# Kernel optimization log

Hardware: AMD Instinct MI355X
Metric: run time of the kernel (lower is better)

The kernel has to match this reference:

```python
import jax, jax.numpy as jnp
import numpy as np

LMAX = 10
F_IN = 64
F_OUT = 64
N_GRID = 512
IRREP_DIM = sum((2 * l + 1) ** 2 for l in range(LMAX + 1))  # 1771
BATCH = 256


def setup_inputs() -> dict:
    key = jax.random.key(0)
    kx, kD, kw = jax.random.split(key, 3)
    x = jax.random.normal(kx, (BATCH, F_IN, IRREP_DIM), dtype=jnp.float32)
    D = jax.random.normal(kD, (N_GRID, IRREP_DIM), dtype=jnp.float32)
    w = jax.random.normal(kw, (F_IN, F_OUT, N_GRID), dtype=jnp.float32)
    return {"x": x, "D": D, "w": w}


def _so3_linear(x, psi):
    # x:   (B, f_in, sum_l (2l+1)^2) signal over SO(3) irreps
    # psi: (f_in, f_out, sum_l (2l+1)^2) per-degree block weights
    B, f_in, _ = x.shape
    f_out = psi.shape[1]
    outs = []
    off = 0
    for l in range(LMAX + 1):
        d = 2 * l + 1
        blk = d * d
        # input block: multiplicity u (=d) x irrep component m (=d)
        x_l = x[:, :, off:off + blk].reshape(B, f_in, d, d)        # (B,i,u,m)
        w_l = psi[:, :, off:off + blk].reshape(f_in, f_out, d, d)  # (i,o,u,v)
        alpha = 1.0 / np.sqrt(f_in * d)  # e3nn fan-in path normalization
        out_l = jnp.einsum('bium,iouv->bovm', x_l, w_l) * alpha
        outs.append(out_l.reshape(B, f_out, blk))
        off += blk
    return jnp.concatenate(outs, axis=-1)


def reference(x, D, w):
    # project spatial filter into Fourier (irrep) domain
    n_grid = D.shape[0]
    psi = jnp.einsum('ni,xyn->xyi', D, w) / np.sqrt(n_grid)  # (f_in, f_out, IRREP_DIM)
    return _so3_linear(x, psi)
```

## Files before the change

kernel.cpp:

```cpp
#include <hip/hip_runtime.h>
#include <hip/hip_bf16.h>

#define IDIM 1771
#define NF 64
#define NG 512

constexpr int OFFS[12] = {0, 1, 10, 35, 84, 165, 286, 455, 680, 969, 1330, 1771};

typedef float f32x4 __attribute__((ext_vector_type(4)));
typedef float f32x2 __attribute__((ext_vector_type(2)));
typedef __bf16 bf16x2 __attribute__((ext_vector_type(2)));
typedef __bf16 bf16x8 __attribute__((ext_vector_type(8)));

__device__ __forceinline__ void gl_lds16(const void* g, void* l) {
    __builtin_amdgcn_global_load_lds((const __attribute__((address_space(1))) void*)g,
                                     (__attribute__((address_space(3))) void*)l, 16, 0, 0);
}

__global__ __launch_bounds__(256) void prep_repack_kernel(const float* __restrict__ D,
                                                          const float* __restrict__ w,
                                                          const float* __restrict__ x,
                                                          __bf16* __restrict__ Dt,
                                                          __bf16* __restrict__ wb,
                                                          __hip_bfloat16* __restrict__ A) {
    __shared__ alignas(16) char smem[16640];
    const int blk = blockIdx.x;
    const int t = threadIdx.x;
    const int lane = t & 63, grp = t >> 6;

    if (blk < 224) {
        float (*T)[65] = (float (*)[65])smem;
        const int ct = blk >> 3, nt = blk & 7;
        const int c0 = ct * 64, n0 = nt * 64;
        float tmp[16];
#pragma unroll
        for (int p = 0; p < 16; ++p) {
            int nn = grp + p * 4;
            int c = c0 + lane;
            tmp[p] = (c < IDIM) ? D[(size_t)(n0 + nn) * IDIM + c] : 0.0f;
        }
#pragma unroll
        for (int p = 0; p < 16; ++p) T[grp + p * 4][lane] = tmp[p];
        __syncthreads();
        for (int cc = grp; cc < 64; cc += 4) {
            int c = c0 + cc;
            if (c < IDIM) Dt[c * NG + n0 + lane] = (__bf16)T[lane][cc];
        }
    } else if (blk < 288) {
        const int o = blk - 224;
#pragma unroll
        for (int ii0 = 0; ii0 < 64; ii0 += 8) {
            f32x2 tmp[8];
#pragma unroll
            for (int j = 0; j < 8; ++j)
                tmp[j] = *(const f32x2*)&w[((size_t)((ii0 + j) * 64 + o)) * NG + t * 2];
#pragma unroll
            for (int j = 0; j < 8; ++j) {
                bf16x2 ov;
                ov.x = (__bf16)tmp[j].x;
                ov.y = (__bf16)tmp[j].y;
                *(bf16x2*)&wb[((size_t)(o * 64 + ii0 + j)) * NG + t * 2] = ov;
            }
        }
    } else {
        const int idx = blk - 288;
        const int l = idx >> 8;
        const int b = idx & 255;
        const int d = 2 * l + 1, off = OFFS[l], csq = d * d, Kp = 64 * d;
        __bf16 (*T)[66] = (__bf16 (*)[66])smem;
        const float* xb = x + (size_t)b * NF * IDIM + off;
        __bf16* Ab = (__bf16*)(A + (size_t)16384 * off + (size_t)b * d * Kp);

        for (int c0 = 0; c0 < csq; c0 += 64) {
            float tmp[16];
#pragma unroll
            for (int p = 0; p < 16; ++p) {
                int ii = grp + p * 4;
                int c = c0 + lane;
                tmp[p] = (c < csq) ? xb[(size_t)ii * IDIM + c] : 0.0f;
            }
#pragma unroll
            for (int p = 0; p < 16; ++p) T[grp + p * 4][lane] = (__bf16)tmp[p];
            __syncthreads();
#pragma unroll
            for (int s = 0; s < 2; ++s) {
                int idx2 = s * 256 + t;
                int c_loc = idx2 >> 3, i0 = (idx2 & 7) * 8;
                int c = c0 + c_loc;
                if (c < csq) {
                    int u = (unsigned)c / (unsigned)d;
                    int m = c - u * d;
                    bf16x8 v;
#pragma unroll
                    for (int j = 0; j < 8; ++j) v[j] = T[i0 + j][c_loc];
                    *(bf16x8*)(Ab + (size_t)m * Kp + u * 64 + i0) = v;
                }
            }
            __syncthreads();
        }
    }
}

__global__ __launch_bounds__(256) void psi_mfma_kernel(const __bf16* __restrict__ Dt,
                                                       const __bf16* __restrict__ wb,
                                                       __bf16* __restrict__ Bm) {
    __shared__ alignas(16) __bf16 S[3 * 8192];

    const int t = threadIdx.x, w = t >> 6, ln = t & 63;
    const int row0 = blockIdx.x * 128;
    const int col0 = blockIdx.y * 128;

    const __bf16* gp[4];
    __bf16* lp[4];
#pragma unroll
    for (int q = 0; q < 4; ++q) {
        int chunk = w * 4 + q;
        bool isA = chunk < 8;
        int j = chunk & 7;
        int r16 = j * 16 + (ln >> 2);
        int g = isA ? (row0 + r16 < IDIM ? row0 + r16 : IDIM - 1) : (col0 + r16);
        gp[q] = (isA ? Dt : wb) + (size_t)g * NG + (ln & 3) * 8;
        lp[q] = S + (isA ? 0 : 4096) + j * 512;
    }

    f32x4 acc[4][4];
    f32x4 zero = {0.0f, 0.0f, 0.0f, 0.0f};
#pragma unroll
    for (int i = 0; i < 4; ++i)
#pragma unroll
        for (int j = 0; j < 4; ++j) acc[i][j] = zero;

    const int wr = (w >> 1) * 64, wc = (w & 1) * 64;
    const int fr = ln & 15, kh = ln >> 4;

    auto STAGE = [&](int bi) {
#pragma unroll
        for (int q = 0; q < 4; ++q) {
            gl_lds16(gp[q], lp[q] + bi * 8192);
            gp[q] += 32;
        }
    };

    const int nsteps = NG / 32;
    STAGE(0);
    STAGE(1);

    int bi = 0;
    for (int s = 0; s < nsteps; ++s) {
        if (s + 1 < nsteps) asm volatile("s_waitcnt vmcnt(4)" ::: "memory");
        else                asm volatile("s_waitcnt vmcnt(0)" ::: "memory");
        __builtin_amdgcn_s_barrier();
        __builtin_amdgcn_sched_barrier(0);
        if (s + 2 < nsteps) {
            int nb = s + 2 - ((s + 2) >= 3 ? 3 : 0);
            nb = (s + 2) % 3;
            STAGE(nb);
        }
        __builtin_amdgcn_sched_barrier(0);
        const __bf16* As_ = S + bi * 8192;
        const __bf16* Bs_ = S + bi * 8192 + 4096;
        bf16x8 af[4], bfr[4];
#pragma unroll
        for (int mt = 0; mt < 4; ++mt)
            af[mt] = *(const bf16x8*)&As_[(wr + mt * 16 + fr) * 32 + kh * 8];
#pragma unroll
        for (int nt = 0; nt < 4; ++nt)
            bfr[nt] = *(const bf16x8*)&Bs_[(wc + nt * 16 + fr) * 32 + kh * 8];
#pragma unroll
        for (int mt = 0; mt < 4; ++mt)
#pragma unroll
            for (int nt = 0; nt < 4; ++nt)
                acc[mt][nt] = __builtin_amdgcn_mfma_f32_16x16x32_bf16(af[mt], bfr[nt],
                                                                      acc[mt][nt], 0, 0, 0);
        bi = (bi == 2) ? 0 : bi + 1;
    }

    const float sc = 0.04419417382415922f;
    const int o = (col0 + wc) >> 6;
#pragma unroll
    for (int mt = 0; mt < 4; ++mt) {
#pragma unroll
        for (int e = 0; e < 4; ++e) {
            int c = row0 + wr + mt * 16 + kh * 4 + e;
            if (c < IDIM) {
                int l = 0;
#pragma unroll
                for (int ll = 1; ll < 11; ++ll)
                    if (c >= OFFS[ll]) l = ll;
                int d = 2 * l + 1, off = OFFS[l];
                int rem = c - off;
                int u = (unsigned)rem / (unsigned)d;
                int v = rem - u * d;
                __bf16* bb = Bm + (size_t)4096 * off + (size_t)(o * d + v) * (64 * d) + u * 64;
#pragma unroll
                for (int nt = 0; nt < 4; ++nt) {
                    int i = nt * 16 + fr;
                    bb[i] = (__bf16)(acc[mt][nt][e] * sc);
                }
            }
        }
    }
}

__global__ __launch_bounds__(256) void so3_gemm_all(const __bf16* __restrict__ A,
                                                    const __bf16* __restrict__ Bm,
                                                    float* __restrict__ out) {
    const int bid = blockIdx.x;
    const int v_ = (bid & 7) * 237 + (bid >> 3);
    if (v_ >= 1892) return;

    int l = 10, base = 0;
    if (v_ >= 462)  { l = 9; base = 462; }
    if (v_ >= 842)  { l = 8; base = 842; }
    if (v_ >= 1148) { l = 7; base = 1148; }
    if (v_ >= 1388) { l = 6; base = 1388; }
    if (v_ >= 1570) { l = 5; base = 1570; }
    if (v_ >= 1702) { l = 4; base = 1702; }
    if (v_ >= 1792) { l = 3; base = 1792; }
    if (v_ >= 1848) { l = 2; base = 1848; }
    if (v_ >= 1878) { l = 1; base = 1878; }
    if (v_ >= 1890) { l = 0; base = 1890; }

    const int d = 2 * l + 1;
    const int off = OFFS[l];
    const int Np = 64 * d, Kp = 64 * d;
    const int ntiles = l + 1;
    const int rel = v_ - base;
    const int bx = (unsigned)rel / (unsigned)ntiles;
    const int by = rel - bx * ntiles;
    const int row0 = bx * 128, col0 = by * 128;

    constexpr float ALPHA[11] = {0.125f, 0.07216878f, 0.05590170f, 0.04724556f,
                                 0.04166667f, 0.03768892f, 0.03466879f, 0.03227486f,
                                 0.03031695f, 0.02867697f, 0.02727724f};

    __shared__ alignas(16) __bf16 S[3 * 8192];

    const int t = threadIdx.x, w = t >> 6, ln = t & 63;

    const __bf16* Abase = A + (size_t)16384 * off;
    const __bf16* Bbase = Bm + (size_t)4096 * off;

    const __bf16* gp[4];
    __bf16* lp[4];
#pragma unroll
    for (int q = 0; q < 4; ++q) {
        int chunk = w * 4 + q;
        bool isA = chunk < 8;
        int j = chunk & 7;
        int r16 = j * 16 + (ln >> 2);
        int g = isA ? (row0 + r16) : (col0 + r16 < Np ? col0 + r16 : Np - 1);
        gp[q] = (isA ? Abase : Bbase) + (size_t)g * Kp + (ln & 3) * 8;
        lp[q] = S + (isA ? 0 : 4096) + j * 512;
    }

    f32x4 acc[4][4];
    f32x4 zero = {0.0f, 0.0f, 0.0f, 0.0f};
#pragma unroll
    for (int i = 0; i < 4; ++i)
#pragma unroll
        for (int j = 0; j < 4; ++j) acc[i][j] = zero;

    const int wr = (w >> 1) * 64, wc = (w & 1) * 64;
    const int fr = ln & 15, kh = ln >> 4;

    auto STAGE = [&](int bi) {
#pragma unroll
        for (int q = 0; q < 4; ++q) {
            gl_lds16(gp[q], lp[q] + bi * 8192);
            gp[q] += 32;
        }
    };

    const int nsteps = Kp / 32;
    STAGE(0);
    STAGE(1);

    int bi = 0;
    for (int s = 0; s < nsteps; ++s) {
        if (s + 1 < nsteps) asm volatile("s_waitcnt vmcnt(4)" ::: "memory");
        else                asm volatile("s_waitcnt vmcnt(0)" ::: "memory");
        __builtin_amdgcn_s_barrier();
        __builtin_amdgcn_sched_barrier(0);
        if (s + 2 < nsteps) STAGE((s + 2) % 3);
        __builtin_amdgcn_sched_barrier(0);
        const __bf16* As_ = S + bi * 8192;
        const __bf16* Bs_ = S + bi * 8192 + 4096;
        bf16x8 af[4], bfr[4];
#pragma unroll
        for (int mt = 0; mt < 4; ++mt)
            af[mt] = *(const bf16x8*)&As_[(wr + mt * 16 + fr) * 32 + kh * 8];
#pragma unroll
        for (int nt = 0; nt < 4; ++nt)
            bfr[nt] = *(const bf16x8*)&Bs_[(wc + nt * 16 + fr) * 32 + kh * 8];
#pragma unroll
        for (int mt = 0; mt < 4; ++mt)
#pragma unroll
            for (int nt = 0; nt < 4; ++nt)
                acc[mt][nt] = __builtin_amdgcn_mfma_f32_16x16x32_bf16(af[mt], bfr[nt],
                                                                      acc[mt][nt], 0, 0, 0);
        bi = (bi == 2) ? 0 : bi + 1;
    }

    __syncthreads();
    float* Tw = (float*)S + w * 256;
    const float alpha = ALPHA[l];

#pragma unroll
    for (int mt = 0; mt < 4; ++mt) {
        int r = row0 + wr + mt * 16 + fr;
        int b = (unsigned)r / (unsigned)d;
        int m = r - b * d;
        float* ob = out + (size_t)b * NF * IDIM + off + m;
#pragma unroll
        for (int nt = 0; nt < 4; ++nt) {
#pragma unroll
            for (int e = 0; e < 4; ++e) Tw[(kh * 4 + e) * 16 + fr] = acc[mt][nt][e];
            f32x4 vals = *(const f32x4*)&Tw[fr * 16 + kh * 4];
            int qb = col0 + wc + nt * 16 + kh * 4;
            int o = (unsigned)qb / (unsigned)d;
            int vv = qb - o * d;
#pragma unroll
            for (int j = 0; j < 4; ++j) {
                if (qb + j < Np) ob[o * IDIM + vv * d] = alpha * vals[j];
                ++vv;
                if (vv == d) { vv = 0; ++o; }
            }
        }
    }
}

extern "C" void kernel_launch(void* const* d_in, const int* in_sizes, int n_in,
                              void* d_out, int out_size, void* d_ws, size_t ws_size,
                              hipStream_t stream) {
    const float* x = (const float*)d_in[0];
    const float* D = (const float*)d_in[1];
    const float* w = (const float*)d_in[2];
    float* out = (float*)d_out;

    char* ws = (char*)d_ws;
    const size_t DT_BYTES = (size_t)IDIM * NG * 2;
    const size_t WB_BYTES = (size_t)4096 * NG * 2;
    const size_t A_BYTES = (size_t)16384 * IDIM * 2;

    __bf16* Dt = (__bf16*)ws;
    __bf16* wb = (__bf16*)(ws + DT_BYTES);
    __hip_bfloat16* A = (__hip_bfloat16*)(ws + DT_BYTES + WB_BYTES);
    __bf16* Bm = (__bf16*)(ws + DT_BYTES + WB_BYTES + A_BYTES);

    prep_repack_kernel<<<3104, 256, 0, stream>>>(D, w, x, Dt, wb, A);
    psi_mfma_kernel<<<dim3(14, 32), 256, 0, stream>>>(Dt, wb, Bm);
    so3_gemm_all<<<1896, 256, 0, stream>>>((const __bf16*)A, Bm, out);
}
```

Measured before the change: 392.4 us.

## Use BK=64 double-buffered XOR-swizzled LDS tiles and split prep kernel

Both MFMA GEMM kernels change from a 3-stage, K=32 pipeline to a 2-stage double buffer with K=64 tiles. The LDS layout uses an XOR swizzle to avoid bank conflicts on 16-byte fragment reads, and waves split loading so two waves load A and two load B. This halves the number of barriers per K while raising LDS use to 64KB per block, which may lower occupancy. The fused prep kernel is also split into a D/w conversion kernel and a separate x repack kernel, so each has its own LDS footprint.

```diff
diff --git a/kernel.cpp b/kernel.cpp
--- a/kernel.cpp
+++ b/kernel.cpp
@@ -17,19 +17,16 @@
                                      (__attribute__((address_space(3))) void*)l, 16, 0, 0);
 }
 
-__global__ __launch_bounds__(256) void prep_repack_kernel(const float* __restrict__ D,
-                                                          const float* __restrict__ w,
-                                                          const float* __restrict__ x,
-                                                          __bf16* __restrict__ Dt,
-                                                          __bf16* __restrict__ wb,
-                                                          __hip_bfloat16* __restrict__ A) {
-    __shared__ alignas(16) char smem[16640];
+__global__ __launch_bounds__(256) void prep_dw_kernel(const float* __restrict__ D,
+                                                      const float* __restrict__ w,
+                                                      __bf16* __restrict__ Dt,
+                                                      __bf16* __restrict__ wb) {
+    __shared__ alignas(16) float T[64][65];
     const int blk = blockIdx.x;
     const int t = threadIdx.x;
     const int lane = t & 63, grp = t >> 6;
 
     if (blk < 224) {
-        float (*T)[65] = (float (*)[65])smem;
         const int ct = blk >> 3, nt = blk & 7;
         const int c0 = ct * 64, n0 = nt * 64;
         float tmp[16];
@@ -46,7 +43,7 @@
             int c = c0 + cc;
             if (c < IDIM) Dt[c * NG + n0 + lane] = (__bf16)T[lane][cc];
         }
-    } else if (blk < 288) {
+    } else {
         const int o = blk - 224;
 #pragma unroll
         for (int ii0 = 0; ii0 < 64; ii0 += 8) {
@@ -62,65 +59,73 @@
                 *(bf16x2*)&wb[((size_t)(o * 64 + ii0 + j)) * NG + t * 2] = ov;
             }
         }
-    } else {
-        const int idx = blk - 288;
-        const int l = idx >> 8;
-        const int b = idx & 255;
-        const int d = 2 * l + 1, off = OFFS[l], csq = d * d, Kp = 64 * d;
-        __bf16 (*T)[66] = (__bf16 (*)[66])smem;
-        const float* xb = x + (size_t)b * NF * IDIM + off;
-        __bf16* Ab = (__bf16*)(A + (size_t)16384 * off + (size_t)b * d * Kp);
-
-        for (int c0 = 0; c0 < csq; c0 += 64) {
-            float tmp[16];
-#pragma unroll
-            for (int p = 0; p < 16; ++p) {
-                int ii = grp + p * 4;
-                int c = c0 + lane;
-                tmp[p] = (c < csq) ? xb[(size_t)ii * IDIM + c] : 0.0f;
-            }
-#pragma unroll
-            for (int p = 0; p < 16; ++p) T[grp + p * 4][lane] = (__bf16)tmp[p];
-            __syncthreads();
-#pragma unroll
-            for (int s = 0; s < 2; ++s) {
-                int idx2 = s * 256 + t;
-                int c_loc = idx2 >> 3, i0 = (idx2 & 7) * 8;
-                int c = c0 + c_loc;
-                if (c < csq) {
-                    int u = (unsigned)c / (unsigned)d;
-                    int m = c - u * d;
-                    bf16x8 v;
-#pragma unroll
-                    for (int j = 0; j < 8; ++j) v[j] = T[i0 + j][c_loc];
-                    *(bf16x8*)(Ab + (size_t)m * Kp + u * 64 + i0) = v;
-                }
-            }
-            __syncthreads();
-        }
+    }
+}
+
+__global__ __launch_bounds__(256) void repack_x_kernel(const float* __restrict__ x,
+                                                       __hip_bfloat16* __restrict__ A) {
+    __shared__ alignas(16) __bf16 T[64][66];
+    const int idx = blockIdx.x;
+    const int l = idx >> 8;
+    const int b = idx & 255;
+    const int t = threadIdx.x;
+    const int lane = t & 63, grp = t >> 6;
+    const int d = 2 * l + 1, off = OFFS[l], csq = d * d, Kp = 64 * d;
+    const float* xb = x + (size_t)b * NF * IDIM + off;
+    __bf16* Ab = (__bf16*)(A + (size_t)16384 * off + (size_t)b * d * Kp);
+
+    for (int c0 = 0; c0 < csq; c0 += 64) {
+        float tmp[16];
+#pragma unroll
+        for (int p = 0; p < 16; ++p) {
+            int ii = grp + p * 4;
+            int c = c0 + lane;
+            tmp[p] = (c < csq) ? xb[(size_t)ii * IDIM + c] : 0.0f;
+        }
+#pragma unroll
+        for (int p = 0; p < 16; ++p) T[grp + p * 4][lane] = (__bf16)tmp[p];
+        __syncthreads();
+#pragma unroll
+        for (int s = 0; s < 2; ++s) {
+            int idx2 = s * 256 + t;
+            int c_loc = idx2 >> 3, i0 = (idx2 & 7) * 8;
+            int c = c0 + c_loc;
+            if (c < csq) {
+                int u = (unsigned)c / (unsigned)d;
+                int m = c - u * d;
+                bf16x8 v;
+#pragma unroll
+                for (int j = 0; j < 8; ++j) v[j] = T[i0 + j][c_loc];
+                *(bf16x8*)(Ab + (size_t)m * Kp + u * 64 + i0) = v;
+            }
+        }
+        __syncthreads();
     }
 }
 
 __global__ __launch_bounds__(256) void psi_mfma_kernel(const __bf16* __restrict__ Dt,
                                                        const __bf16* __restrict__ wb,
                                                        __bf16* __restrict__ Bm) {
-    __shared__ alignas(16) __bf16 S[3 * 8192];
+    __shared__ alignas(16) __bf16 S[2 * 16384];
 
     const int t = threadIdx.x, w = t >> 6, ln = t & 63;
     const int row0 = blockIdx.x * 128;
     const int col0 = blockIdx.y * 128;
 
-    const __bf16* gp[4];
-    __bf16* lp[4];
-#pragma unroll
-    for (int q = 0; q < 4; ++q) {
-        int chunk = w * 4 + q;
-        bool isA = chunk < 8;
-        int j = chunk & 7;
-        int r16 = j * 16 + (ln >> 2);
-        int g = isA ? (row0 + r16 < IDIM ? row0 + r16 : IDIM - 1) : (col0 + r16);
-        gp[q] = (isA ? Dt : wb) + (size_t)g * NG + (ln & 3) * 8;
-        lp[q] = S + (isA ? 0 : 4096) + j * 512;
+    const bool isA = (w < 2);
+    const int wsub = w & 1;
+    const int rowloc = ln >> 3;
+    const int logslot = (ln & 7) ^ rowloc;
+
+    const __bf16* gp[8];
+    __bf16* lp[8];
+#pragma unroll
+    for (int q = 0; q < 8; ++q) {
+        int chunk = wsub * 8 + q;
+        int row = chunk * 8 + rowloc;
+        int g = isA ? (row0 + row < IDIM ? row0 + row : IDIM - 1) : (col0 + row);
+        gp[q] = (isA ? Dt : wb) + (size_t)g * NG + logslot * 8;
+        lp[q] = S + (isA ? 0 : 8192) + chunk * 512;
     }
 
     f32x4 acc[4][4];
@@ -132,47 +137,56 @@
 
     const int wr = (w >> 1) * 64, wc = (w & 1) * 64;
     const int fr = ln & 15, kh = ln >> 4;
-
-    auto STAGE = [&](int bi) {
-#pragma unroll
-        for (int q = 0; q < 4; ++q) {
-            gl_lds16(gp[q], lp[q] + bi * 8192);
-            gp[q] += 32;
-        }
-    };
-
-    const int nsteps = NG / 32;
-    STAGE(0);
-    STAGE(1);
+    const int fx = fr & 7;
+
+    int aoff[2][4], boff[2][4];
+#pragma unroll
+    for (int kk = 0; kk < 2; ++kk)
+#pragma unroll
+        for (int mt = 0; mt < 4; ++mt) {
+            aoff[kk][mt] = (wr + mt * 16 + fr) * 64 + (((kk << 2) | kh) ^ fx) * 8;
+            boff[kk][mt] = (wc + mt * 16 + fr) * 64 + (((kk << 2) | kh) ^ fx) * 8;
+        }
+
+    const int np = NG / 64;
+
+#pragma unroll
+    for (int q = 0; q < 8; ++q) { gl_lds16(gp[q], lp[q]); gp[q] += 64; }
+    asm volatile("s_waitcnt vmcnt(0)" ::: "memory");
+    __builtin_amdgcn_s_barrier();
+    __builtin_amdgcn_sched_barrier(0);
 
     int bi = 0;
-    for (int s = 0; s < nsteps; ++s) {
-        if (s + 1 < nsteps) asm volatile("s_waitcnt vmcnt(4)" ::: "memory");
-        else                asm volatile("s_waitcnt vmcnt(0)" ::: "memory");
+    for (int p = 0; p < np; ++p) {
+        if (p + 1 < np) {
+#pragma unroll
+            for (int q = 0; q < 8; ++q) {
+                gl_lds16(gp[q], lp[q] + (bi ^ 1) * 16384);
+                gp[q] += 64;
+            }
+        }
+        const __bf16* As_ = S + bi * 16384;
+        const __bf16* Bs_ = As_ + 8192;
+        bf16x8 af[2][4], bf_[2][4];
+#pragma unroll
+        for (int kk = 0; kk < 2; ++kk) {
+#pragma unroll
+            for (int mt = 0; mt < 4; ++mt) af[kk][mt] = *(const bf16x8*)&As_[aoff[kk][mt]];
+#pragma unroll
+            for (int nt = 0; nt < 4; ++nt) bf_[kk][nt] = *(const bf16x8*)&Bs_[boff[kk][nt]];
+        }
+#pragma unroll
+        for (int kk = 0; kk < 2; ++kk)
+#pragma unroll
+            for (int mt = 0; mt < 4; ++mt)
+#pragma unroll
+                for (int nt = 0; nt < 4; ++nt)
+                    acc[mt][nt] = __builtin_amdgcn_mfma_f32_16x16x32_bf16(
+                        af[kk][mt], bf_[kk][nt], acc[mt][nt], 0, 0, 0);
+        asm volatile("s_waitcnt vmcnt(0)" ::: "memory");
         __builtin_amdgcn_s_barrier();
         __builtin_amdgcn_sched_barrier(0);
-        if (s + 2 < nsteps) {
-            int nb = s + 2 - ((s + 2) >= 3 ? 3 : 0);
-            nb = (s + 2) % 3;
-            STAGE(nb);
-        }
-        __builtin_amdgcn_sched_barrier(0);
-        const __bf16* As_ = S + bi * 8192;
-        const __bf16* Bs_ = S + bi * 8192 + 4096;
-        bf16x8 af[4], bfr[4];
-#pragma unroll
-        for (int mt = 0; mt < 4; ++mt)
-            af[mt] = *(const bf16x8*)&As_[(wr + mt * 16 + fr) * 32 + kh * 8];
-#pragma unroll
-        for (int nt = 0; nt < 4; ++nt)
-            bfr[nt] = *(const bf16x8*)&Bs_[(wc + nt * 16 + fr) * 32 + kh * 8];
-#pragma unroll
-        for (int mt = 0; mt < 4; ++mt)
-#pragma unroll
-            for (int nt = 0; nt < 4; ++nt)
-                acc[mt][nt] = __builtin_amdgcn_mfma_f32_16x16x32_bf16(af[mt], bfr[nt],
-                                                                      acc[mt][nt], 0, 0, 0);
-        bi = (bi == 2) ? 0 : bi + 1;
+        bi ^= 1;
     }
 
     const float sc = 0.04419417382415922f;
@@ -234,24 +248,27 @@
                                  0.04166667f, 0.03768892f, 0.03466879f, 0.03227486f,
                                  0.03031695f, 0.02867697f, 0.02727724f};
 
-    __shared__ alignas(16) __bf16 S[3 * 8192];
+    __shared__ alignas(16) __bf16 S[2 * 16384];
 
     const int t = threadIdx.x, w = t >> 6, ln = t & 63;
 
     const __bf16* Abase = A + (size_t)16384 * off;
     const __bf16* Bbase = Bm + (size_t)4096 * off;
 
-    const __bf16* gp[4];
-    __bf16* lp[4];
-#pragma unroll
-    for (int q = 0; q < 4; ++q) {
-        int chunk = w * 4 + q;
-        bool isA = chunk < 8;
-        int j = chunk & 7;
-        int r16 = j * 16 + (ln >> 2);
-        int g = isA ? (row0 + r16) : (col0 + r16 < Np ? col0 + r16 : Np - 1);
-        gp[q] = (isA ? Abase : Bbase) + (size_t)g * Kp + (ln & 3) * 8;
-        lp[q] = S + (isA ? 0 : 4096) + j * 512;
+    const bool isA = (w < 2);
+    const int wsub = w & 1;
+    const int rowloc = ln >> 3;
+    const int logslot = (ln & 7) ^ rowloc;
+
+    const __bf16* gp[8];
+    __bf16* lp[8];
+#pragma unroll
+    for (int q = 0; q < 8; ++q) {
+        int chunk = wsub * 8 + q;
+        int row = chunk * 8 + rowloc;
+        int g = isA ? (row0 + row) : (col0 + row < Np ? col0 + row : Np - 1);
+        gp[q] = (isA ? Abase : Bbase) + (size_t)g * Kp + logslot * 8;
+        lp[q] = S + (isA ? 0 : 8192) + chunk * 512;
     }
 
     f32x4 acc[4][4];
@@ -263,43 +280,56 @@
 
     const int wr = (w >> 1) * 64, wc = (w & 1) * 64;
     const int fr = ln & 15, kh = ln >> 4;
-
-    auto STAGE = [&](int bi) {
-#pragma unroll
-        for (int q = 0; q < 4; ++q) {
-            gl_lds16(gp[q], lp[q] + bi * 8192);
-            gp[q] += 32;
-        }
-    };
-
-    const int nsteps = Kp / 32;
-    STAGE(0);
-    STAGE(1);
+    const int fx = fr & 7;
+
+    int aoff[2][4], boff[2][4];
+#pragma unroll
+    for (int kk = 0; kk < 2; ++kk)
+#pragma unroll
+        for (int mt = 0; mt < 4; ++mt) {
+            aoff[kk][mt] = (wr + mt * 16 + fr) * 64 + (((kk << 2) | kh) ^ fx) * 8;
+            boff[kk][mt] = (wc + mt * 16 + fr) * 64 + (((kk << 2) | kh) ^ fx) * 8;
+        }
+
+    const int np = Kp / 64;
+
+#pragma unroll
+    for (int q = 0; q < 8; ++q) { gl_lds16(gp[q], lp[q]); gp[q] += 64; }
+    asm volatile("s_waitcnt vmcnt(0)" ::: "memory");
+    __builtin_amdgcn_s_barrier();
+    __builtin_amdgcn_sched_barrier(0);
 
     int bi = 0;
-    for (int s = 0; s < nsteps; ++s) {
-        if (s + 1 < nsteps) asm volatile("s_waitcnt vmcnt(4)" ::: "memory");
-        else                asm volatile("s_waitcnt vmcnt(0)" ::: "memory");
+    for (int p = 0; p < np; ++p) {
+        if (p + 1 < np) {
+#pragma unroll
+            for (int q = 0; q < 8; ++q) {
+                gl_lds16(gp[q], lp[q] + (bi ^ 1) * 16384);
+                gp[q] += 64;
+            }
+        }
+        const __bf16* As_ = S + bi * 16384;
+        const __bf16* Bs_ = As_ + 8192;
+        bf16x8 af[2][4], bf_[2][4];
+#pragma unroll
+        for (int kk = 0; kk < 2; ++kk) {
+#pragma unroll
+            for (int mt = 0; mt < 4; ++mt) af[kk][mt] = *(const bf16x8*)&As_[aoff[kk][mt]];
+#pragma unroll
+            for (int nt = 0; nt < 4; ++nt) bf_[kk][nt] = *(const bf16x8*)&Bs_[boff[kk][nt]];
+        }
+#pragma unroll
+        for (int kk = 0; kk < 2; ++kk)
+#pragma unroll
+            for (int mt = 0; mt < 4; ++mt)
+#pragma unroll
+                for (int nt = 0; nt < 4; ++nt)
+                    acc[mt][nt] = __builtin_amdgcn_mfma_f32_16x16x32_bf16(
+                        af[kk][mt], bf_[kk][nt], acc[mt][nt], 0, 0, 0);
+        asm volatile("s_waitcnt vmcnt(0)" ::: "memory");
         __builtin_amdgcn_s_barrier();
         __builtin_amdgcn_sched_barrier(0);
-        if (s + 2 < nsteps) STAGE((s + 2) % 3);
-        __builtin_amdgcn_sched_barrier(0);
-        const __bf16* As_ = S + bi * 8192;
-        const __bf16* Bs_ = S + bi * 8192 + 4096;
-        bf16x8 af[4], bfr[4];
-#pragma unroll
-        for (int mt = 0; mt < 4; ++mt)
-            af[mt] = *(const bf16x8*)&As_[(wr + mt * 16 + fr) * 32 + kh * 8];
-#pragma unroll
-        for (int nt = 0; nt < 4; ++nt)
-            bfr[nt] = *(const bf16x8*)&Bs_[(wc + nt * 16 + fr) * 32 + kh * 8];
-#pragma unroll
-        for (int mt = 0; mt < 4; ++mt)
-#pragma unroll
-            for (int nt = 0; nt < 4; ++nt)
-                acc[mt][nt] = __builtin_amdgcn_mfma_f32_16x16x32_bf16(af[mt], bfr[nt],
-                                                                      acc[mt][nt], 0, 0, 0);
-        bi = (bi == 2) ? 0 : bi + 1;
+        bi ^= 1;
     }
 
     __syncthreads();
@@ -348,7 +378,8 @@
     __hip_bfloat16* A = (__hip_bfloat16*)(ws + DT_BYTES + WB_BYTES);
     __bf16* Bm = (__bf16*)(ws + DT_BYTES + WB_BYTES + A_BYTES);
 
-    prep_repack_kernel<<<3104, 256, 0, stream>>>(D, w, x, Dt, wb, A);
+    prep_dw_kernel<<<288, 256, 0, stream>>>(D, w, Dt, wb);
+    repack_x_kernel<<<2816, 256, 0, stream>>>(x, A);
     psi_mfma_kernel<<<dim3(14, 32), 256, 0, stream>>>(Dt, wb, Bm);
     so3_gemm_all<<<1896, 256, 0, stream>>>((const __bf16*)A, Bm, out);
 }
```

Result: faster. 379.5 us (-3.3%).
